# Kernel tuning notes

Hardware: AMD Instinct MI355X
Metric: run time of the kernel (lower is better)

Reference implementation:

```python
import jax, jax.numpy as jnp
import numpy as np

FEAT_DIM = 48        # feature_dim init arg
C_OUT = 2 * FEAT_DIM # conv output channels -> table row width
H = W_IMG = 256      # image spatial size -> res = C_OUT*H*W / (2*FEAT_DIM) = 65536
N_PTS = 2_000_000    # query points


def setup_inputs() -> dict:
    key = jax.random.key(0)
    k1, k2, k3, k4 = jax.random.split(key, 4)
    pts = jax.random.uniform(k1, (N_PTS, 2), dtype=jnp.float32)  # coords in [0,1)
    image = jax.random.normal(k2, (1, 3, H, W_IMG), dtype=jnp.float32)
    conv_w = jax.random.normal(k3, (C_OUT, 3, 3, 3), dtype=jnp.float32) * 0.05
    conv_b = jax.random.normal(k4, (C_OUT,), dtype=jnp.float32) * 0.05
    return {"pts": pts, "image": image, "conv_w": conv_w, "conv_b": conv_b}


def reference(pts, image, conv_w, conv_b):
    # feature_extractor: Conv2d(3, 96, k=3, SAME) -> [1, 96, 256, 256]
    feat = jax.lax.conv_general_dilated(
        image, conv_w, window_strides=(1, 1), padding="SAME",
        dimension_numbers=("NCHW", "OIHW", "NCHW"))
    feat = feat + conv_b[None, :, None, None]
    fa = feat.reshape(-1, 2 * FEAT_DIM)  # [res, 96]
    res = fa.shape[0]                    # 65536

    x = pts[:, 0] * (res - 1)
    y = pts[:, 1] * (res - 1)
    hi = res - 1 - 1e-5
    x1 = jnp.floor(jnp.clip(x, 0, hi)).astype(jnp.int32)
    y1 = jnp.floor(jnp.clip(y, 0, hi)).astype(jnp.int32)
    x2 = jnp.clip(x1 + 1, 0, res - 1)
    y2 = jnp.clip(y1 + 1, 0, res - 1)

    xw1 = (x2.astype(x.dtype) - x)[:, None]
    xw2 = (x - x1.astype(x.dtype))[:, None]
    yw1 = (y2.astype(y.dtype) - y)[:, None]
    yw2 = (y - y1.astype(y.dtype))[:, None]

    fx = fa[:, :FEAT_DIM]  # x-array half of the dual array
    fy = fa[:, FEAT_DIM:]  # y-array half
    # four gathers + weighted blend -> [N, FEAT_DIM]
    return xw1 * fx[x1] + xw2 * fx[x2] + yw1 * fy[y1] + yw2 * fy[y2]
```

## Files before the change

### kernel.cpp

```cpp
#include <hip/hip_runtime.h>
#include <hip/hip_bf16.h>

#define C_OUT 96
#define FEAT_DIM 48
#define HW 256
#define NPIX 65536
#define RES 65536
#define IMG_C 3

typedef __attribute__((ext_vector_type(2))) float f32x2;
typedef __attribute__((ext_vector_type(4))) float f32x4;
typedef __attribute__((ext_vector_type(8))) unsigned short u16x8;
typedef __attribute__((ext_vector_type(4))) unsigned short u16x4;

static __device__ __forceinline__ unsigned short f2bf(float f) {
    unsigned u = __float_as_uint(f);
    u += 0x7fffu + ((u >> 16) & 1u);
    return (unsigned short)(u >> 16);
}
static __device__ __forceinline__ float bf2f(unsigned short h) {
    return __uint_as_float(((unsigned)h) << 16);
}

__global__ __launch_bounds__(256) void conv_kernel(
    const float* __restrict__ img,
    const float* __restrict__ w,
    const float* __restrict__ b,
    unsigned short* __restrict__ FX,
    unsigned short* __restrict__ FY)
{
    __shared__ float ws[C_OUT * 27];
    __shared__ float bs[C_OUT];
    for (int i = threadIdx.x; i < C_OUT * 27; i += blockDim.x) ws[i] = w[i];
    for (int i = threadIdx.x; i < C_OUT; i += blockDim.x) bs[i] = b[i];
    __syncthreads();

    int tid = blockIdx.x * blockDim.x + threadIdx.x;
    if (tid >= (C_OUT * NPIX) / 4) return;
    int f = tid << 2;
    int c  = f >> 16;
    int p  = f & 65535;
    int h  = p >> 8;
    int wc = p & 255;

    float a0 = bs[c], a1 = a0, a2 = a0, a3 = a0;
#pragma unroll
    for (int ci = 0; ci < IMG_C; ++ci) {
        const float* ip = img + ci * NPIX;
#pragma unroll
        for (int kh = 0; kh < 3; ++kh) {
            int hh = h + kh - 1;
            if ((unsigned)hh >= 256u) continue;
            const float* row = ip + hh * HW;
            float win[6];
#pragma unroll
            for (int k = 0; k < 6; ++k) {
                int ww = wc + k - 1;
                win[k] = ((unsigned)ww < 256u) ? row[ww] : 0.0f;
            }
            const float* wk = &ws[c * 27 + ci * 9 + kh * 3];
#pragma unroll
            for (int kw = 0; kw < 3; ++kw) {
                float wt = wk[kw];
                a0 = fmaf(win[kw + 0], wt, a0);
                a1 = fmaf(win[kw + 1], wt, a1);
                a2 = fmaf(win[kw + 2], wt, a2);
                a3 = fmaf(win[kw + 3], wt, a3);
            }
        }
    }

    int r = (unsigned)f / 96u;
    int j = f - r * 96;
    u16x4 pk;
    pk.x = f2bf(a0); pk.y = f2bf(a1); pk.z = f2bf(a2); pk.w = f2bf(a3);
    unsigned short* dst = (j < FEAT_DIM)
        ? (FX + (size_t)r * FEAT_DIM + j)
        : (FY + (size_t)r * FEAT_DIM + (j - FEAT_DIM));
    *(u16x4*)dst = pk;
}

__global__ __launch_bounds__(256) void interp_kernel(
    const float* __restrict__ pts,
    const unsigned short* __restrict__ FX,
    const unsigned short* __restrict__ FY,
    float* __restrict__ out,
    int npts)
{
    int t = blockIdx.x * blockDim.x + threadIdx.x;
    int pt = t / 6;
    int q  = t - pt * 6;
    if (pt >= npts) return;

    f32x2 p = __builtin_nontemporal_load((const f32x2*)pts + pt);

    float x = fminf(fmaxf(p.x * 65535.0f, 0.0f), 65535.0f);
    float y = fminf(fmaxf(p.y * 65535.0f, 0.0f), 65535.0f);

    int x1 = (int)x;
    int y1 = (int)y;
    int x2 = min(x1 + 1, RES - 1);
    int y2 = min(y1 + 1, RES - 1);

    float xw1 = (float)x2 - x;
    float xw2 = x - (float)x1;
    float yw1 = (float)y2 - y;
    float yw2 = y - (float)y1;

    int qo = q * 8;
    const u16x8 A = *(const u16x8*)(FX + (size_t)x1 * FEAT_DIM + qo);
    const u16x8 B = *(const u16x8*)(FX + (size_t)x2 * FEAT_DIM + qo);
    const u16x8 C = *(const u16x8*)(FY + (size_t)y1 * FEAT_DIM + qo);
    const u16x8 D = *(const u16x8*)(FY + (size_t)y2 * FEAT_DIM + qo);

    float o[8];
#pragma unroll
    for (int k = 0; k < 8; ++k) {
        o[k] = xw1 * bf2f(A[k]) + xw2 * bf2f(B[k])
             + yw1 * bf2f(C[k]) + yw2 * bf2f(D[k]);
    }

    float* op = out + (size_t)pt * FEAT_DIM + qo;
    f32x4 v0 = {o[0], o[1], o[2], o[3]};
    f32x4 v1 = {o[4], o[5], o[6], o[7]};
    *(f32x4*)op = v0;
    *(f32x4*)(op + 4) = v1;
}

extern "C" void kernel_launch(void* const* d_in, const int* in_sizes, int n_in,
                              void* d_out, int out_size, void* d_ws, size_t ws_size,
                              hipStream_t stream) {
    const float* pts    = (const float*)d_in[0];
    const float* image  = (const float*)d_in[1];
    const float* conv_w = (const float*)d_in[2];
    const float* conv_b = (const float*)d_in[3];
    float* out = (float*)d_out;

    unsigned short* FX = (unsigned short*)d_ws;
    unsigned short* FY = FX + (size_t)RES * FEAT_DIM;

    int npts = in_sizes[0] / 2;

    {
        int total = (C_OUT * NPIX) / 4;
        int blocks = (total + 255) / 256;
        conv_kernel<<<blocks, 256, 0, stream>>>(image, conv_w, conv_b, FX, FY);
    }
    {
        long long total = (long long)npts * 6;
        int blocks = (int)((total + 255) / 256);
        interp_kernel<<<blocks, 256, 0, stream>>>(pts, FX, FY, out, npts);
    }
}
```

Before: 238.3 us.

## Quantize feature tables to int8 with per-row scales for gathers

Adds a quantization pass that turns the bf16 feature tables into int8 rows with one float scale per row. The interpolation kernel then gathers 16 int8 values per thread instead of 8 bf16 values and folds the row scale into the blend weights. Each point now uses 3 threads instead of 6. The aim is to halve gather traffic and table footprint so the tables fit better in cache, at the cost of two extra kernel launches, extra scale loads, and coarser precision that may exceed the accuracy tolerance.

```diff
diff --git a/kernel.cpp b/kernel.cpp
--- a/kernel.cpp
+++ b/kernel.cpp
@@ -12,6 +12,7 @@
 typedef __attribute__((ext_vector_type(4))) float f32x4;
 typedef __attribute__((ext_vector_type(8))) unsigned short u16x8;
 typedef __attribute__((ext_vector_type(4))) unsigned short u16x4;
+typedef __attribute__((ext_vector_type(16))) signed char i8x16;
 
 static __device__ __forceinline__ unsigned short f2bf(float f) {
     unsigned u = __float_as_uint(f);
@@ -80,16 +81,56 @@
     *(u16x4*)dst = pk;
 }
 
+__global__ __launch_bounds__(256) void quant_kernel(
+    const unsigned short* __restrict__ F,
+    signed char* __restrict__ Q,
+    float* __restrict__ S,
+    int nrows)
+{
+    int r = blockIdx.x * blockDim.x + threadIdx.x;
+    if (r >= nrows) return;
+    const u16x8* row = (const u16x8*)(F + (size_t)r * FEAT_DIM);
+
+    float v[48];
+    float m = 0.0f;
+#pragma unroll
+    for (int i = 0; i < 6; ++i) {
+        u16x8 h = row[i];
+#pragma unroll
+        for (int k = 0; k < 8; ++k) {
+            float f = bf2f(h[k]);
+            v[i * 8 + k] = f;
+            m = fmaxf(m, fabsf(f));
+        }
+    }
+    float inv = (m > 0.0f) ? 127.0f / m : 0.0f;
+    float s   = m * (1.0f / 127.0f);
+
+    i8x16 o0, o1, o2;
+#pragma unroll
+    for (int k = 0; k < 16; ++k) o0[k] = (signed char)(int)rintf(v[k] * inv);
+#pragma unroll
+    for (int k = 0; k < 16; ++k) o1[k] = (signed char)(int)rintf(v[16 + k] * inv);
+#pragma unroll
+    for (int k = 0; k < 16; ++k) o2[k] = (signed char)(int)rintf(v[32 + k] * inv);
+
+    i8x16* qp = (i8x16*)(Q + (size_t)r * FEAT_DIM);
+    qp[0] = o0; qp[1] = o1; qp[2] = o2;
+    S[r] = s;
+}
+
 __global__ __launch_bounds__(256) void interp_kernel(
     const float* __restrict__ pts,
-    const unsigned short* __restrict__ FX,
-    const unsigned short* __restrict__ FY,
+    const signed char* __restrict__ QX,
+    const signed char* __restrict__ QY,
+    const float* __restrict__ SX,
+    const float* __restrict__ SY,
     float* __restrict__ out,
     int npts)
 {
     int t = blockIdx.x * blockDim.x + threadIdx.x;
-    int pt = t / 6;
-    int q  = t - pt * 6;
+    int pt = t / 3;
+    int q  = t - pt * 3;
     if (pt >= npts) return;
 
     f32x2 p = __builtin_nontemporal_load((const f32x2*)pts + pt);
@@ -107,24 +148,32 @@
     float yw1 = (float)y2 - y;
     float yw2 = y - (float)y1;
 
-    int qo = q * 8;
-    const u16x8 A = *(const u16x8*)(FX + (size_t)x1 * FEAT_DIM + qo);
-    const u16x8 B = *(const u16x8*)(FX + (size_t)x2 * FEAT_DIM + qo);
-    const u16x8 C = *(const u16x8*)(FY + (size_t)y1 * FEAT_DIM + qo);
-    const u16x8 D = *(const u16x8*)(FY + (size_t)y2 * FEAT_DIM + qo);
-
-    float o[8];
-#pragma unroll
-    for (int k = 0; k < 8; ++k) {
-        o[k] = xw1 * bf2f(A[k]) + xw2 * bf2f(B[k])
-             + yw1 * bf2f(C[k]) + yw2 * bf2f(D[k]);
+    int qo = q * 16;
+    const i8x16 A = *(const i8x16*)(QX + (size_t)x1 * FEAT_DIM + qo);
+    const i8x16 B = *(const i8x16*)(QX + (size_t)x2 * FEAT_DIM + qo);
+    const i8x16 C = *(const i8x16*)(QY + (size_t)y1 * FEAT_DIM + qo);
+    const i8x16 D = *(const i8x16*)(QY + (size_t)y2 * FEAT_DIM + qo);
+    float wa = xw1 * SX[x1];
+    float wb = xw2 * SX[x2];
+    float wc = yw1 * SY[y1];
+    float wd = yw2 * SY[y2];
+
+    float o[16];
+#pragma unroll
+    for (int k = 0; k < 16; ++k) {
+        o[k] = wa * (float)A[k] + wb * (float)B[k]
+             + wc * (float)C[k] + wd * (float)D[k];
     }
 
     float* op = out + (size_t)pt * FEAT_DIM + qo;
-    f32x4 v0 = {o[0], o[1], o[2], o[3]};
-    f32x4 v1 = {o[4], o[5], o[6], o[7]};
+    f32x4 v0 = {o[0],  o[1],  o[2],  o[3]};
+    f32x4 v1 = {o[4],  o[5],  o[6],  o[7]};
+    f32x4 v2 = {o[8],  o[9],  o[10], o[11]};
+    f32x4 v3 = {o[12], o[13], o[14], o[15]};
     *(f32x4*)op = v0;
-    *(f32x4*)(op + 4) = v1;
+    *(f32x4*)(op + 4)  = v1;
+    *(f32x4*)(op + 8)  = v2;
+    *(f32x4*)(op + 12) = v3;
 }
 
 extern "C" void kernel_launch(void* const* d_in, const int* in_sizes, int n_in,
@@ -136,19 +185,25 @@
     const float* conv_b = (const float*)d_in[3];
     float* out = (float*)d_out;
 
-    unsigned short* FX = (unsigned short*)d_ws;
+    char* wsb = (char*)d_ws;
+    unsigned short* FX = (unsigned short*)wsb;
     unsigned short* FY = FX + (size_t)RES * FEAT_DIM;
+    signed char* QX = (signed char*)(wsb + 2 * (size_t)RES * FEAT_DIM * 2);
+    signed char* QY = QX + (size_t)RES * FEAT_DIM;
+    float* SX = (float*)(QY + (size_t)RES * FEAT_DIM);
+    float* SY = SX + RES;
 
     int npts = in_sizes[0] / 2;
 
     {
         int total = (C_OUT * NPIX) / 4;
-        int blocks = (total + 255) / 256;
-        conv_kernel<<<blocks, 256, 0, stream>>>(image, conv_w, conv_b, FX, FY);
-    }
+        conv_kernel<<<(total + 255) / 256, 256, 0, stream>>>(image, conv_w, conv_b, FX, FY);
+    }
+    quant_kernel<<<RES / 256, 256, 0, stream>>>(FX, QX, SX, RES);
+    quant_kernel<<<RES / 256, 256, 0, stream>>>(FY, QY, SY, RES);
     {
-        long long total = (long long)npts * 6;
+        long long total = (long long)npts * 3;
         int blocks = (int)((total + 255) / 256);
-        interp_kernel<<<blocks, 256, 0, stream>>>(pts, FX, FY, out, npts);
-    }
-}
+        interp_kernel<<<blocks, 256, 0, stream>>>(pts, QX, QY, SX, SY, out, npts);
+    }
+}
```

Measured after the change: 243.4 us. +2.1%, slower.
